# Kernel optimization log

Hardware: AMD Instinct MI355X
Metric: run time of the kernel (lower is better)

Reference implementation:

```python
import jax, jax.numpy as jnp
import numpy as np

N_NODES = 100000
N_EDGES = 3200000
IN_FEAT = 256
OUT_FEAT = 128

def setup_inputs() -> dict:
    key = jax.random.key(0)
    k1, k2, k3, k4, k5 = jax.random.split(key, 5)
    feat = jax.random.normal(k1, (N_NODES, IN_FEAT), dtype=jnp.float32)
    edge_row = jnp.sort(jax.random.randint(k2, (N_EDGES,), 0, N_NODES, dtype=jnp.int32))
    edge_col = jax.random.randint(k3, (N_EDGES,), 0, N_NODES, dtype=jnp.int32)
    edge_val = jax.random.uniform(k4, (N_EDGES,), dtype=jnp.float32)
    # Xavier-uniform init like the torch module
    limit = float(np.sqrt(6.0 / (IN_FEAT + OUT_FEAT)))
    weight = jax.random.uniform(k5, (IN_FEAT, OUT_FEAT), dtype=jnp.float32, minval=-limit, maxval=limit)
    return {"feat": feat, "edge_row": edge_row, "edge_col": edge_col, "edge_val": edge_val, "weight": weight}

def reference(feat, edge_row, edge_col, edge_val, weight):
    # feat_embedding = feat @ W            [N, out_feat]
    feat_embedding = jnp.matmul(feat, weight)
    # x = spmm(adj, feat_embedding): out[i] = sum_{edges e: row[e]=i} val[e] * femb[col[e]]
    messages = edge_val[:, None] * feat_embedding[edge_col]  # [E, out_feat]
    x = jax.ops.segment_sum(messages, edge_row, num_segments=N_NODES)
    return (feat_embedding, x)
```

## Files before the change

### kernel.cpp

```cpp
#include <hip/hip_runtime.h>
#include <hip/hip_fp16.h>

#define IN_FEAT 256
#define OUT_FEAT 128

typedef _Float16 half8 __attribute__((ext_vector_type(8)));
typedef _Float16 half4 __attribute__((ext_vector_type(4)));
typedef float    f32x4 __attribute__((ext_vector_type(4)));

#define WT_BYTES (OUT_FEAT * IN_FEAT * 2)

__global__ __launch_bounds__(256) void wprep_kernel(
    const float* __restrict__ W, char* __restrict__ wt)
{
    int t   = blockIdx.x * blockDim.x + threadIdx.x;
    int col = t & 127;
    int k   = (t >> 7) * 2;
    _Float16 h0 = (_Float16)W[(size_t)k       * OUT_FEAT + col];
    _Float16 h1 = (_Float16)W[(size_t)(k + 1) * OUT_FEAT + col];
    int byte = col * 512 + k * 2;
    byte ^= (col & 7) << 4;
    unsigned short u0, u1;
    __builtin_memcpy(&u0, &h0, 2);
    __builtin_memcpy(&u1, &h1, 2);
    *(unsigned int*)(wt + byte) = (unsigned int)u0 | ((unsigned int)u1 << 16);
}

#define GBM 128
#define GT  512

__global__ __launch_bounds__(GT, 1) void gemm_mfma_kernel(
    const float* __restrict__ A, const char* __restrict__ wt,
    float* __restrict__ C, __half* __restrict__ Ch, int M, int writeHalf)
{
    __shared__ _Float16 sA[GBM * IN_FEAT];
    __shared__ _Float16 sW[OUT_FEAT * IN_FEAT];

    const int t    = threadIdx.x;
    const int row0 = blockIdx.x * GBM;

    {
        const int row = t >> 2;
        const int kq  = t & 3;
        int grow = row0 + row; if (grow >= M) grow = M - 1;
        const float* Ap = &A[(size_t)grow * IN_FEAT];
        #pragma unroll
        for (int i = 0; i < 8; ++i) {
            int k = kq * 8 + i * 32;
            float4 a0 = *(const float4*)(Ap + k);
            float4 a1 = *(const float4*)(Ap + k + 4);
            half8 h;
            h[0]=(_Float16)a0.x; h[1]=(_Float16)a0.y; h[2]=(_Float16)a0.z; h[3]=(_Float16)a0.w;
            h[4]=(_Float16)a1.x; h[5]=(_Float16)a1.y; h[6]=(_Float16)a1.z; h[7]=(_Float16)a1.w;
            int byte = row * 512 + k * 2;
            byte ^= (row & 7) << 4;
            *(half8*)((char*)sA + byte) = h;
        }
    }
    {
        const float4* src = (const float4*)wt;
        float4*       dst = (float4*)sW;
        #pragma unroll
        for (int i = 0; i < 8; ++i) dst[t + GT * i] = src[t + GT * i];
    }
    __syncthreads();

    const int wid  = t >> 6;
    const int lane = t & 63;
    const int rowBase = wid * 16;
    const int fr = lane & 15;
    const int fk = lane >> 4;

    f32x4 acc[8];
    #pragma unroll
    for (int nt = 0; nt < 8; ++nt) acc[nt] = (f32x4){0.f, 0.f, 0.f, 0.f};

    #pragma unroll
    for (int ks = 0; ks < 8; ++ks) {
        const int arow  = rowBase + fr;
        int abyte = arow * 512 + ks * 64 + fk * 16;
        abyte ^= (arow & 7) << 4;
        half8 af = *(const half8*)((const char*)sA + abyte);
        #pragma unroll
        for (int nt = 0; nt < 8; ++nt) {
            const int col = nt * 16 + fr;
            int bbyte = col * 512 + ks * 64 + fk * 16;
            bbyte ^= (col & 7) << 4;
            half8 bf = *(const half8*)((const char*)sW + bbyte);
            acc[nt] = __builtin_amdgcn_mfma_f32_16x16x32_f16(bf, af, acc[nt], 0, 0, 0);
        }
    }

    const int grow = row0 + rowBase + fr;
    if (grow < M) {
        #pragma unroll
        for (int nt = 0; nt < 8; ++nt) {
            const int col0 = nt * 16 + fk * 4;
            float4 o = {acc[nt][0], acc[nt][1], acc[nt][2], acc[nt][3]};
            *(float4*)&C[(size_t)grow * OUT_FEAT + col0] = o;
            if (writeHalf) {
                half4 h = {(_Float16)o.x, (_Float16)o.y, (_Float16)o.z, (_Float16)o.w};
                *(half4*)&Ch[(size_t)grow * OUT_FEAT + col0] = h;
            }
        }
    }
}

__global__ void zero_kernel(float4* __restrict__ p, int n4)
{
    int i      = blockIdx.x * blockDim.x + threadIdx.x;
    int stride = gridDim.x * blockDim.x;
    for (; i < n4; i += stride) p[i] = float4{0.f, 0.f, 0.f, 0.f};
}

#define EPB 512
#define EPW 128
#define PF  16

template<int USE_H>
__global__ __launch_bounds__(256) void spmm_kernel(
    const int*   __restrict__ erow, const int* __restrict__ ecol,
    const float* __restrict__ eval, const float* __restrict__ femb,
    const __half* __restrict__ fembh, float* __restrict__ x, int E)
{
    __shared__ int   s_row[EPB];
    __shared__ int   s_col[EPB];
    __shared__ float s_val[EPB];

    const int blockBase = blockIdx.x * EPB;

    #pragma unroll
    for (int i = 0; i < 2; ++i) {
        int li = threadIdx.x + i * 256;
        int e  = blockBase + li;
        if (e < E) {
            s_row[li] = __builtin_nontemporal_load(&erow[e]);
            s_col[li] = __builtin_nontemporal_load(&ecol[e]);
            s_val[li] = __builtin_nontemporal_load(&eval[e]);
        }
    }
    __syncthreads();

    const int wave = threadIdx.x >> 6;
    const int lane = threadIdx.x & 63;
    const int j    = lane * 2;

    const int w0 = wave * EPW;
    const int g0 = blockBase + w0;
    if (g0 >= E) return;
    const int n = min(EPW, E - g0);

    float2 acc = {0.f, 0.f};
    int cur = s_row[w0];

    if (n == EPW) {
        #pragma unroll 1
        for (int base = 0; base < EPW; base += PF) {
            __half2 h[PF];
            float2  f[PF];
            if constexpr (USE_H) {
                #pragma unroll
                for (int i = 0; i < PF; ++i) {
                    int c = s_col[w0 + base + i];
                    h[i] = *(const __half2*)&fembh[(size_t)c * OUT_FEAT + j];
                }
            } else {
                #pragma unroll
                for (int i = 0; i < PF; ++i) {
                    int c = s_col[w0 + base + i];
                    f[i] = *(const float2*)&femb[(size_t)c * OUT_FEAT + j];
                }
            }
            #pragma unroll
            for (int i = 0; i < PF; ++i) {
                int r = s_row[w0 + base + i];
                if (r != cur) {
                    atomicAdd(&x[(size_t)cur * OUT_FEAT + j],     acc.x);
                    atomicAdd(&x[(size_t)cur * OUT_FEAT + j + 1], acc.y);
                    acc.x = 0.f; acc.y = 0.f;
                    cur = r;
                }
                float v = s_val[w0 + base + i];
                float2 fv;
                if constexpr (USE_H) fv = __half22float2(h[i]); else fv = f[i];
                acc.x = fmaf(v, fv.x, acc.x);
                acc.y = fmaf(v, fv.y, acc.y);
            }
        }
    } else {
        for (int idx = 0; idx < n; ++idx) {
            int r = s_row[w0 + idx];
            if (r != cur) {
                atomicAdd(&x[(size_t)cur * OUT_FEAT + j],     acc.x);
                atomicAdd(&x[(size_t)cur * OUT_FEAT + j + 1], acc.y);
                acc.x = 0.f; acc.y = 0.f;
                cur = r;
            }
            int c = s_col[w0 + idx];
            float v = s_val[w0 + idx];
            float2 fv;
            if constexpr (USE_H) fv = __half22float2(*(const __half2*)&fembh[(size_t)c * OUT_FEAT + j]);
            else                 fv = *(const float2*)&femb[(size_t)c * OUT_FEAT + j];
            acc.x = fmaf(v, fv.x, acc.x);
            acc.y = fmaf(v, fv.y, acc.y);
        }
    }
    atomicAdd(&x[(size_t)cur * OUT_FEAT + j],     acc.x);
    atomicAdd(&x[(size_t)cur * OUT_FEAT + j + 1], acc.y);
}

extern "C" void kernel_launch(void* const* d_in, const int* in_sizes, int n_in,
                              void* d_out, int out_size, void* d_ws, size_t ws_size,
                              hipStream_t stream)
{
    const float* feat = (const float*)d_in[0];
    const int*   erow = (const int*)  d_in[1];
    const int*   ecol = (const int*)  d_in[2];
    const float* eval = (const float*)d_in[3];
    const float* W    = (const float*)d_in[4];

    const int M = in_sizes[0] / IN_FEAT;
    const int E = in_sizes[1];

    float*  femb  = (float*)d_out;
    float*  x     = femb + (size_t)M * OUT_FEAT;
    char*   wt    = (char*)d_ws;
    __half* fembh = (__half*)((char*)d_ws + WT_BYTES);

    const size_t needH = (size_t)WT_BYTES + (size_t)M * OUT_FEAT * sizeof(__half);
    const int useH = (ws_size >= needH) ? 1 : 0;

    wprep_kernel<<<64, 256, 0, stream>>>(W, wt);

    gemm_mfma_kernel<<<(M + GBM - 1) / GBM, GT, 0, stream>>>(feat, wt, femb, fembh, M, useH);

    zero_kernel<<<2048, 256, 0, stream>>>((float4*)x, (M * OUT_FEAT) / 4);

    int nblk = (E + EPB - 1) / EPB;
    if (useH) spmm_kernel<1><<<nblk, 256, 0, stream>>>(erow, ecol, eval, femb, fembh, x, E);
    else      spmm_kernel<0><<<nblk, 256, 0, stream>>>(erow, ecol, eval, femb, fembh, x, E);
}
```

Before: 359.5 us.

## Split each wave into two half-waves processing edge pairs with 4-wide gathers

The SpMM kernel now has each half-wave (32 lanes) handle a different edge of a pair, with each lane gathering 4 contiguous features (half4/float4) instead of 2. Partial sums from the two halves are combined with a cross-half shuffle before the atomic adds, and row boundaries inside a pair are handled by masking values per half. This widens each gather and halves the number of serial loop iterations per wave. In exchange it adds shuffles at every flush and extra branching when a row boundary falls inside a pair.

```diff
diff --git a/kernel.cpp b/kernel.cpp
--- a/kernel.cpp
+++ b/kernel.cpp
@@ -115,7 +115,7 @@
 
 #define EPB 512
 #define EPW 128
-#define PF  16
+#define PPB 16
 
 template<int USE_H>
 __global__ __launch_bounds__(256) void spmm_kernel(
@@ -143,70 +143,106 @@
 
     const int wave = threadIdx.x >> 6;
     const int lane = threadIdx.x & 63;
-    const int j    = lane * 2;
+    const int q    = lane & 31;
+    const int hi   = lane >> 5;
+    const int c0   = q * 4;
 
     const int w0 = wave * EPW;
     const int g0 = blockBase + w0;
     if (g0 >= E) return;
     const int n = min(EPW, E - g0);
 
-    float2 acc = {0.f, 0.f};
+    float4 acc = {0.f, 0.f, 0.f, 0.f};
     int cur = s_row[w0];
+
+    auto flushAcc = [&](int row) {
+        float4 o;
+        o.x = __shfl_xor(acc.x, 32);
+        o.y = __shfl_xor(acc.y, 32);
+        o.z = __shfl_xor(acc.z, 32);
+        o.w = __shfl_xor(acc.w, 32);
+        if (lane < 32) {
+            float* xp = &x[(size_t)row * OUT_FEAT + c0];
+            atomicAdd(xp + 0, acc.x + o.x);
+            atomicAdd(xp + 1, acc.y + o.y);
+            atomicAdd(xp + 2, acc.z + o.z);
+            atomicAdd(xp + 3, acc.w + o.w);
+        }
+        acc.x = 0.f; acc.y = 0.f; acc.z = 0.f; acc.w = 0.f;
+    };
+
+    auto consumePair = [&](int p, float4 f, bool hasOdd) {
+        int   r0 = s_row[p];
+        int   r1 = hasOdd ? s_row[p + 1] : r0;
+        float v  = (hi && !hasOdd) ? 0.f : s_val[p + (hasOdd ? hi : 0)];
+        if (r0 != cur) { flushAcc(cur); cur = r0; }
+        if (r1 == r0) {
+            acc.x = fmaf(v, f.x, acc.x);
+            acc.y = fmaf(v, f.y, acc.y);
+            acc.z = fmaf(v, f.z, acc.z);
+            acc.w = fmaf(v, f.w, acc.w);
+        } else {
+            float v0 = hi ? 0.f : v;
+            acc.x = fmaf(v0, f.x, acc.x);
+            acc.y = fmaf(v0, f.y, acc.y);
+            acc.z = fmaf(v0, f.z, acc.z);
+            acc.w = fmaf(v0, f.w, acc.w);
+            flushAcc(cur);
+            cur = r1;
+            float v1 = hi ? v : 0.f;
+            acc.x = fmaf(v1, f.x, acc.x);
+            acc.y = fmaf(v1, f.y, acc.y);
+            acc.z = fmaf(v1, f.z, acc.z);
+            acc.w = fmaf(v1, f.w, acc.w);
+        }
+    };
 
     if (n == EPW) {
         #pragma unroll 1
-        for (int base = 0; base < EPW; base += PF) {
-            __half2 h[PF];
-            float2  f[PF];
+        for (int base = 0; base < EPW; base += 2 * PPB) {
+            half4  hb[PPB];
+            float4 fb[PPB];
             if constexpr (USE_H) {
                 #pragma unroll
-                for (int i = 0; i < PF; ++i) {
-                    int c = s_col[w0 + base + i];
-                    h[i] = *(const __half2*)&fembh[(size_t)c * OUT_FEAT + j];
+                for (int i = 0; i < PPB; ++i) {
+                    int c = s_col[w0 + base + 2 * i + hi];
+                    hb[i] = *(const half4*)&fembh[(size_t)c * OUT_FEAT + c0];
                 }
             } else {
                 #pragma unroll
-                for (int i = 0; i < PF; ++i) {
-                    int c = s_col[w0 + base + i];
-                    f[i] = *(const float2*)&femb[(size_t)c * OUT_FEAT + j];
+                for (int i = 0; i < PPB; ++i) {
+                    int c = s_col[w0 + base + 2 * i + hi];
+                    fb[i] = *(const float4*)&femb[(size_t)c * OUT_FEAT + c0];
                 }
             }
             #pragma unroll
-            for (int i = 0; i < PF; ++i) {
-                int r = s_row[w0 + base + i];
-                if (r != cur) {
-                    atomicAdd(&x[(size_t)cur * OUT_FEAT + j],     acc.x);
-                    atomicAdd(&x[(size_t)cur * OUT_FEAT + j + 1], acc.y);
-                    acc.x = 0.f; acc.y = 0.f;
-                    cur = r;
-                }
-                float v = s_val[w0 + base + i];
-                float2 fv;
-                if constexpr (USE_H) fv = __half22float2(h[i]); else fv = f[i];
-                acc.x = fmaf(v, fv.x, acc.x);
-                acc.y = fmaf(v, fv.y, acc.y);
+            for (int i = 0; i < PPB; ++i) {
+                float4 f;
+                if constexpr (USE_H) {
+                    f.x = (float)hb[i][0]; f.y = (float)hb[i][1];
+                    f.z = (float)hb[i][2]; f.w = (float)hb[i][3];
+                } else f = fb[i];
+                consumePair(w0 + base + 2 * i, f, true);
             }
         }
     } else {
-        for (int idx = 0; idx < n; ++idx) {
-            int r = s_row[w0 + idx];
-            if (r != cur) {
-                atomicAdd(&x[(size_t)cur * OUT_FEAT + j],     acc.x);
-                atomicAdd(&x[(size_t)cur * OUT_FEAT + j + 1], acc.y);
-                acc.x = 0.f; acc.y = 0.f;
-                cur = r;
-            }
-            int c = s_col[w0 + idx];
-            float v = s_val[w0 + idx];
-            float2 fv;
-            if constexpr (USE_H) fv = __half22float2(*(const __half2*)&fembh[(size_t)c * OUT_FEAT + j]);
-            else                 fv = *(const float2*)&femb[(size_t)c * OUT_FEAT + j];
-            acc.x = fmaf(v, fv.x, acc.x);
-            acc.y = fmaf(v, fv.y, acc.y);
-        }
-    }
-    atomicAdd(&x[(size_t)cur * OUT_FEAT + j],     acc.x);
-    atomicAdd(&x[(size_t)cur * OUT_FEAT + j + 1], acc.y);
+        for (int base = 0; base < n; base += 2) {
+            bool hasOdd = (base + 1) < n;
+            int  p  = w0 + base;
+            int  pe = p + (hasOdd ? hi : 0);
+            int  c  = s_col[pe];
+            float4 f;
+            if constexpr (USE_H) {
+                half4 h = *(const half4*)&fembh[(size_t)c * OUT_FEAT + c0];
+                f.x = (float)h[0]; f.y = (float)h[1];
+                f.z = (float)h[2]; f.w = (float)h[3];
+            } else {
+                f = *(const float4*)&femb[(size_t)c * OUT_FEAT + c0];
+            }
+            consumePair(p, f, hasOdd);
+        }
+    }
+    flushAcc(cur);
 }
 
 extern "C" void kernel_launch(void* const* d_in, const int* in_sizes, int n_in,
```

Measured after the change: 461.1 us. +28.3%, slower.
